# Optimization experiments

Measured on AMD Instinct MI355X. Metric: run time of the kernel, lower is better.

The kernel has to match this reference:

```python
import jax, jax.numpy as jnp
import numpy as np

N_SRC = 50000
N_DST = 50000
N_EDGES = 800000
D = 128
H = 128


def setup_inputs() -> dict:
    key = jax.random.key(0)
    ks = jax.random.split(key, 10)
    return {
        "feat_src": jax.random.normal(ks[0], (N_SRC, D), dtype=jnp.float32),
        "feat_dst": jax.random.normal(ks[1], (N_DST, D), dtype=jnp.float32),
        "W1": jax.random.normal(ks[2], (H, D), dtype=jnp.float32) * 0.05,
        "b1": jnp.zeros((H,), dtype=jnp.float32),
        "W2": jax.random.normal(ks[3], (H, 3 * D), dtype=jnp.float32) * 0.05,
        "b2": jnp.zeros((H,), dtype=jnp.float32),
        "W3": jax.random.normal(ks[4], (H, 2 * H), dtype=jnp.float32) * 0.05,
        "b3": jnp.zeros((H,), dtype=jnp.float32),
        "src_idx": jax.random.randint(ks[5], (N_EDGES,), 0, N_SRC, dtype=jnp.int32),
        "dst_idx": jax.random.randint(ks[6], (N_EDGES,), 0, N_DST, dtype=jnp.int32),
    }


def reference(feat_src, feat_dst, W1, b1, W2, b2, W3, b3, src_idx, dst_idx):
    n_dst = feat_dst.shape[0]
    # copy_u: gather source features along edges  [E, D]
    m = feat_src[src_idx]
    # fn.max -> 'max'; NOTE: source code's 'mean' is ALSO fn.max (faithful to bug)
    mx = jax.ops.segment_max(m, dst_idx, num_segments=n_dst)
    mx = jnp.where(jnp.isfinite(mx), mx, jnp.zeros_like(mx))  # zero-degree dst -> 0 (DGL convention)
    sm = jax.ops.segment_sum(m, dst_idx, num_segments=n_dst)
    agg = jnp.concatenate([mx, mx, sm], axis=1)  # [N_dst, 3D]
    z2 = agg @ W2.T + b2            # fc2
    z1 = feat_dst @ W1.T + b1       # fc1
    h = jax.nn.relu(jnp.concatenate([z2, z1], axis=1))  # [N_dst, 2H]
    out = jax.nn.relu(h @ W3.T + b3)  # fc3 = Linear + ReLU
    return out
```

## Files before the change

### kernel.cpp

```cpp
#include <hip/hip_runtime.h>
#include <math.h>

#define NDST 50000
#define NSRC 50000
#define NEDGE 800000
#define DF 128

#define NBUK 1563
#define NCH 128
#define EPC (NEDGE / NCH)
#define HN (NBUK * NCH)
#define CAP 1536

typedef __attribute__((ext_vector_type(4))) float f32x4;
typedef __attribute__((ext_vector_type(8))) short bf16x8;

__device__ __forceinline__ ushort f2bf(float f) {
    union { float f; unsigned int u; } c; c.f = f;
    unsigned int u = c.u;
    unsigned int r = (u + 0x7fffu + ((u >> 16) & 1u)) >> 16;
    return (ushort)r;
}
__device__ __forceinline__ float bflo(unsigned int u) {
    union { unsigned int u; float f; } c; c.u = u << 16; return c.f;
}
__device__ __forceinline__ float bfhi(unsigned int u) {
    union { unsigned int u; float f; } c; c.u = u & 0xffff0000u; return c.f;
}

#define NB_CONV 6250
#define NB_CONVD 6250
#define NB_ZERO 196
#define NB_PREP 320

__global__ void prep_all(const float* __restrict__ fs, unsigned int* __restrict__ fs_b,
                         const float* __restrict__ fd, unsigned int* __restrict__ fd_b,
                         uint4* __restrict__ hist4,
                         const float* __restrict__ W2, const float* __restrict__ W1,
                         const float* __restrict__ W3,
                         ushort* __restrict__ Wz_b, ushort* __restrict__ W1_b,
                         ushort* __restrict__ W3_b) {
    int b = blockIdx.x, tid = threadIdx.x;
    if (b < NB_CONV + NB_CONVD) {
        const float* src = (b < NB_CONV) ? fs : fd;
        unsigned int* dst = (b < NB_CONV) ? fs_b : fd_b;
        int i = ((b < NB_CONV) ? b : b - NB_CONV) * 256 + tid;
        float4 v = *(const float4*)(src + (size_t)i * 4);
        unsigned int lo = (unsigned int)f2bf(v.x) | ((unsigned int)f2bf(v.y) << 16);
        unsigned int hi = (unsigned int)f2bf(v.z) | ((unsigned int)f2bf(v.w) << 16);
        *(uint2*)(dst + (size_t)i * 2) = make_uint2(lo, hi);
    } else if (b < NB_CONV + NB_CONVD + NB_ZERO) {
        int i = (b - NB_CONV - NB_CONVD) * 256 + tid;
        if (i < HN / 4) hist4[i] = make_uint4(0, 0, 0, 0);
    } else {
        int i = (b - NB_CONV - NB_CONVD - NB_ZERO) * 256 + tid;
        if (i < 128 * 256) {
            int c = i >> 8, k = i & 255;
            float v = (k < 128) ? (W2[c * 384 + k] + W2[c * 384 + 128 + k])
                                : W2[c * 384 + 128 + k];
            Wz_b[i] = f2bf(v);
        } else if (i < 128 * 256 + 128 * 128) {
            int j = i - 128 * 256;
            W1_b[j] = f2bf(W1[j]);
        } else if (i < 128 * 256 + 128 * 128 + 128 * 256) {
            int j = i - 128 * 256 - 128 * 128;
            W3_b[j] = f2bf(W3[j]);
        }
    }
}

__global__ void hist_k(const int* __restrict__ dst_idx, int* __restrict__ hist) {
    int c = blockIdx.x, tid = threadIdx.x;
    int base = c * EPC;
    for (int e = base + tid; e < base + EPC; e += 256)
        atomicAdd(&hist[(dst_idx[e] >> 5) * NCH + c], 1);
}

__global__ void scan_bsums(const int* __restrict__ a, int* __restrict__ bsum, int n) {
    __shared__ int ws[4];
    int i = blockIdx.x * 256 + threadIdx.x;
    int v = (i < n) ? a[i] : 0;
    #pragma unroll
    for (int off = 32; off > 0; off >>= 1) v += __shfl_down(v, off, 64);
    if ((threadIdx.x & 63) == 0) ws[threadIdx.x >> 6] = v;
    __syncthreads();
    if (threadIdx.x == 0) bsum[blockIdx.x] = ws[0] + ws[1] + ws[2] + ws[3];
}

__global__ __launch_bounds__(256)
void scan_mid(const int* __restrict__ bsum, int* __restrict__ bpre, int nb) {
    __shared__ int part[256];
    int t = threadIdx.x;
    int ch = (nb + 255) / 256;
    int lo = t * ch, hi = min(nb, lo + ch);
    int s = 0;
    for (int i = lo; i < hi; ++i) s += bsum[i];
    part[t] = s;
    __syncthreads();
    for (int off = 1; off < 256; off <<= 1) {
        int v = (t >= off) ? part[t - off] : 0;
        __syncthreads();
        part[t] += v;
        __syncthreads();
    }
    int run = (t == 0) ? 0 : part[t - 1];
    for (int i = lo; i < hi; ++i) { bpre[i] = run; run += bsum[i]; }
}

__global__ __launch_bounds__(256)
void scan_final(const int* __restrict__ a, const int* __restrict__ bpre,
                int* __restrict__ out, int n) {
    __shared__ int s[256];
    int b = blockIdx.x, t = threadIdx.x;
    int i = b * 256 + t;
    int v = (i < n) ? a[i] : 0;
    s[t] = v;
    __syncthreads();
    for (int off = 1; off < 256; off <<= 1) {
        int u = (t >= off) ? s[t - off] : 0;
        __syncthreads();
        s[t] += u;
        __syncthreads();
    }
    if (i < n) out[i] = bpre[b] + s[t] - v;
}

__global__ __launch_bounds__(256)
void partition_k(const int* __restrict__ src_idx, const int* __restrict__ dst_idx,
                 const int* __restrict__ scanned, unsigned int* __restrict__ pairs) {
    __shared__ int offs_l[NBUK];
    int c = blockIdx.x, tid = threadIdx.x;
    for (int i = tid; i < NBUK; i += 256) offs_l[i] = scanned[i * NCH + c];
    __syncthreads();
    int base = c * EPC;
    for (int e = base + tid; e < base + EPC; e += 256) {
        int d = dst_idx[e];
        int pos = atomicAdd(&offs_l[d >> 5], 1);
        pairs[pos] = (unsigned int)src_idx[e] | ((unsigned int)(d & 31) << 16);
    }
}

__global__ __launch_bounds__(256)
void bucket_sort_agg(const unsigned int* __restrict__ fs_b,
                     const unsigned int* __restrict__ pairs,
                     const int* __restrict__ scanned,
                     unsigned int* __restrict__ mx_b, unsigned int* __restrict__ sm_b) {
    __shared__ int s_src[CAP];
    __shared__ int s_cnt[32], s_off[32], s_cur[32];
    int B = blockIdx.x, tid = threadIdx.x;
    int w = tid >> 6, lane = tid & 63;
    int s0 = scanned[B * NCH];
    int s1 = (B + 1 < NBUK) ? scanned[(B + 1) * NCH] : NEDGE;

    float mx0[8], mx1[8], sm0[8], sm1[8];
    #pragma unroll
    for (int j = 0; j < 8; ++j) {
        mx0[j] = -INFINITY; mx1[j] = -INFINITY; sm0[j] = 0.f; sm1[j] = 0.f;
    }

    for (int cs = s0; cs < s1; cs += CAP) {
        int n = min(CAP, s1 - cs);
        if (tid < 32) s_cnt[tid] = 0;
        __syncthreads();
        for (int i = tid; i < n; i += 256)
            atomicAdd(&s_cnt[(pairs[cs + i] >> 16) & 31u], 1);
        __syncthreads();
        if (tid < 32) {
            int v = s_cnt[tid];
            int incl = v;
            #pragma unroll
            for (int d = 1; d < 32; d <<= 1) {
                int o = __shfl_up(incl, d, 64);
                if (tid >= d) incl += o;
            }
            s_off[tid] = incl - v;
            s_cur[tid] = incl - v;
        }
        __syncthreads();
        for (int i = tid; i < n; i += 256) {
            unsigned int p = pairs[cs + i];
            int pos = atomicAdd(&s_cur[(p >> 16) & 31u], 1);
            s_src[pos] = (int)(p & 0xFFFFu);
        }
        __syncthreads();
        #pragma unroll
        for (int j = 0; j < 8; ++j) {
            int dl = w * 8 + j;
            int e = s_off[dl], eend = e + s_cnt[dl];
            for (; e + 3 < eend; e += 4) {
                int i0 = s_src[e], i1 = s_src[e + 1], i2 = s_src[e + 2], i3 = s_src[e + 3];
                unsigned int u0 = fs_b[(size_t)i0 * 64 + lane];
                unsigned int u1 = fs_b[(size_t)i1 * 64 + lane];
                unsigned int u2 = fs_b[(size_t)i2 * 64 + lane];
                unsigned int u3 = fs_b[(size_t)i3 * 64 + lane];
                float a0 = bflo(u0), c0 = bfhi(u0);
                float a1 = bflo(u1), c1 = bfhi(u1);
                float a2 = bflo(u2), c2 = bfhi(u2);
                float a3 = bflo(u3), c3 = bfhi(u3);
                mx0[j] = fmaxf(fmaxf(fmaxf(mx0[j], a0), a1), fmaxf(a2, a3));
                mx1[j] = fmaxf(fmaxf(fmaxf(mx1[j], c0), c1), fmaxf(c2, c3));
                sm0[j] += (a0 + a1) + (a2 + a3);
                sm1[j] += (c0 + c1) + (c2 + c3);
            }
            for (; e < eend; ++e) {
                unsigned int u = fs_b[(size_t)s_src[e] * 64 + lane];
                float a = bflo(u), c = bfhi(u);
                mx0[j] = fmaxf(mx0[j], a);
                mx1[j] = fmaxf(mx1[j], c);
                sm0[j] += a;
                sm1[j] += c;
            }
        }
        __syncthreads();
    }

    int base_d = B * 32;
    #pragma unroll
    for (int j = 0; j < 8; ++j) {
        int d = base_d + w * 8 + j;
        if (d >= NDST) continue;
        float m0 = mx0[j], m1 = mx1[j];
        if (m0 == -INFINITY) m0 = 0.f;
        if (m1 == -INFINITY) m1 = 0.f;
        union { float f; unsigned int u; } c0, c1;
        c0.f = m0; c1.f = m1;
        size_t o = (size_t)d * 64 + lane;
        mx_b[o] = (c0.u >> 16) | (c1.u & 0xFFFF0000u);
        sm_b[o] = (unsigned int)f2bf(sm0[j]) | ((unsigned int)f2bf(sm1[j]) << 16);
    }
}

#define BM2 64
#define LDH 260

__global__ __launch_bounds__(256)
void mlp_fused(const ushort* __restrict__ mxa, const ushort* __restrict__ sma,
               const ushort* __restrict__ fdb,
               const ushort* __restrict__ Wz_b, const ushort* __restrict__ W1_b,
               const ushort* __restrict__ W3_b,
               const float* __restrict__ b1, const float* __restrict__ b2,
               const float* __restrict__ b3,
               float* __restrict__ out) {
    __shared__ ushort Hs[BM2 * LDH];
    int tid = threadIdx.x;
    int bm = blockIdx.x * BM2;
    int wid = tid >> 6, lane = tid & 63;
    int wm = (wid & 1) * 32, wn = (wid >> 1) * 64;
    int lrow = lane & 15, lk8 = (lane >> 4) * 8;
    int rbase = (lane >> 4) * 4;

    int am0 = min(bm + wm + lrow, NDST - 1);
    int am1 = min(bm + wm + 16 + lrow, NDST - 1);
    int bn[4];
    #pragma unroll
    for (int ni = 0; ni < 4; ++ni) bn[ni] = wn + ni * 16 + lrow;

    f32x4 acc[2][4];

    #pragma unroll
    for (int i = 0; i < 2; ++i)
        #pragma unroll
        for (int j = 0; j < 4; ++j) acc[i][j] = (f32x4){0.f, 0.f, 0.f, 0.f};
    #pragma unroll 2
    for (int k0 = 0; k0 < 256; k0 += 32) {
        const ushort* ap = (k0 < 128) ? mxa : sma;
        int kl = (k0 & 127) + lk8;
        bf16x8 af0 = *(const bf16x8*)(ap + (size_t)am0 * 128 + kl);
        bf16x8 af1 = *(const bf16x8*)(ap + (size_t)am1 * 128 + kl);
        #pragma unroll
        for (int ni = 0; ni < 4; ++ni) {
            bf16x8 bf = *(const bf16x8*)(Wz_b + (size_t)bn[ni] * 256 + k0 + lk8);
            acc[0][ni] = __builtin_amdgcn_mfma_f32_16x16x32_bf16(af0, bf, acc[0][ni], 0, 0, 0);
            acc[1][ni] = __builtin_amdgcn_mfma_f32_16x16x32_bf16(af1, bf, acc[1][ni], 0, 0, 0);
        }
    }
    #pragma unroll
    for (int ni = 0; ni < 4; ++ni) {
        float bv = b2[bn[ni]];
        #pragma unroll
        for (int mi = 0; mi < 2; ++mi)
            #pragma unroll
            for (int r = 0; r < 4; ++r)
                Hs[(wm + mi * 16 + rbase + r) * LDH + bn[ni]] =
                    f2bf(fmaxf(acc[mi][ni][r] + bv, 0.f));
    }

    #pragma unroll
    for (int i = 0; i < 2; ++i)
        #pragma unroll
        for (int j = 0; j < 4; ++j) acc[i][j] = (f32x4){0.f, 0.f, 0.f, 0.f};
    #pragma unroll 2
    for (int k0 = 0; k0 < 128; k0 += 32) {
        bf16x8 af0 = *(const bf16x8*)(fdb + (size_t)am0 * 128 + k0 + lk8);
        bf16x8 af1 = *(const bf16x8*)(fdb + (size_t)am1 * 128 + k0 + lk8);
        #pragma unroll
        for (int ni = 0; ni < 4; ++ni) {
            bf16x8 bf = *(const bf16x8*)(W1_b + (size_t)bn[ni] * 128 + k0 + lk8);
            acc[0][ni] = __builtin_amdgcn_mfma_f32_16x16x32_bf16(af0, bf, acc[0][ni], 0, 0, 0);
            acc[1][ni] = __builtin_amdgcn_mfma_f32_16x16x32_bf16(af1, bf, acc[1][ni], 0, 0, 0);
        }
    }
    #pragma unroll
    for (int ni = 0; ni < 4; ++ni) {
        float bv = b1[bn[ni]];
        #pragma unroll
        for (int mi = 0; mi < 2; ++mi)
            #pragma unroll
            for (int r = 0; r < 4; ++r)
                Hs[(wm + mi * 16 + rbase + r) * LDH + 128 + bn[ni]] =
                    f2bf(fmaxf(acc[mi][ni][r] + bv, 0.f));
    }

    __syncthreads();

    #pragma unroll
    for (int i = 0; i < 2; ++i)
        #pragma unroll
        for (int j = 0; j < 4; ++j) acc[i][j] = (f32x4){0.f, 0.f, 0.f, 0.f};
    #pragma unroll 2
    for (int k0 = 0; k0 < 256; k0 += 32) {
        bf16x8 af0 = *(const bf16x8*)&Hs[(wm + lrow) * LDH + k0 + lk8];
        bf16x8 af1 = *(const bf16x8*)&Hs[(wm + 16 + lrow) * LDH + k0 + lk8];
        #pragma unroll
        for (int ni = 0; ni < 4; ++ni) {
            bf16x8 bf = *(const bf16x8*)(W3_b + (size_t)bn[ni] * 256 + k0 + lk8);
            acc[0][ni] = __builtin_amdgcn_mfma_f32_16x16x32_bf16(af0, bf, acc[0][ni], 0, 0, 0);
            acc[1][ni] = __builtin_amdgcn_mfma_f32_16x16x32_bf16(af1, bf, acc[1][ni], 0, 0, 0);
        }
    }
    #pragma unroll
    for (int ni = 0; ni < 4; ++ni) {
        float bv = b3[bn[ni]];
        #pragma unroll
        for (int mi = 0; mi < 2; ++mi)
            #pragma unroll
            for (int r = 0; r < 4; ++r) {
                int m = bm + wm + mi * 16 + rbase + r;
                if (m < NDST)
                    out[(size_t)m * 128 + bn[ni]] = fmaxf(acc[mi][ni][r] + bv, 0.f);
            }
    }
}

extern "C" void kernel_launch(void* const* d_in, const int* in_sizes, int n_in,
                              void* d_out, int out_size, void* d_ws, size_t ws_size,
                              hipStream_t stream) {
    const float* feat_src = (const float*)d_in[0];
    const float* feat_dst = (const float*)d_in[1];
    const float* W1 = (const float*)d_in[2];
    const float* b1 = (const float*)d_in[3];
    const float* W2 = (const float*)d_in[4];
    const float* b2 = (const float*)d_in[5];
    const float* W3 = (const float*)d_in[6];
    const float* b3 = (const float*)d_in[7];
    const int* src_idx = (const int*)d_in[8];
    const int* dst_idx = (const int*)d_in[9];

    float* out = (float*)d_out;

    unsigned int* fs_b = (unsigned int*)d_ws;
    unsigned int* mx_b = fs_b + (size_t)NSRC * 64;
    unsigned int* sm_b = mx_b + (size_t)NDST * 64;
    unsigned int* fd_b = sm_b + (size_t)NDST * 64;
    ushort* Wz_b = (ushort*)(fd_b + (size_t)NDST * 64);
    ushort* W1_b = Wz_b + 128 * 256;
    ushort* W3_b = W1_b + 128 * 128;
    int* hist    = (int*)(W3_b + 128 * 256);
    int* scanned = hist + HN;
    int* bsum    = scanned + HN;
    int* bpre    = bsum + 1024;
    unsigned int* pairs = (unsigned int*)(bpre + 1024);

    const int NBH = (HN + 255) / 256;

    prep_all<<<NB_CONV + NB_CONVD + NB_ZERO + NB_PREP, 256, 0, stream>>>(
        feat_src, fs_b, feat_dst, fd_b, (uint4*)hist, W2, W1, W3, Wz_b, W1_b, W3_b);

    hist_k<<<NCH, 256, 0, stream>>>(dst_idx, hist);
    scan_bsums<<<NBH, 256, 0, stream>>>(hist, bsum, HN);
    scan_mid<<<1, 256, 0, stream>>>(bsum, bpre, NBH);
    scan_final<<<NBH, 256, 0, stream>>>(hist, bpre, scanned, HN);
    partition_k<<<NCH, 256, 0, stream>>>(src_idx, dst_idx, scanned, pairs);

    bucket_sort_agg<<<NBUK, 256, 0, stream>>>(fs_b, pairs, scanned, mx_b, sm_b);

    mlp_fused<<<(NDST + BM2 - 1) / BM2, 256, 0, stream>>>(
        (const ushort*)mx_b, (const ushort*)sm_b, (const ushort*)fd_b,
        Wz_b, W1_b, W3_b, b1, b2, b3, out);
}
```

Before: 168.2 us.

## Stage MLP weight tiles through LDS with register double-buffered prefetch

Weight K-slices for the three GEMMs in the fused MLP kernel are now loaded cooperatively into a shared-memory tile, one 32-wide slice at a time. The next slice and the next A fragments are prefetched into registers while the current slice is used for MFMAs. This replaces per-wave redundant global loads of weights, which two waves each re-read, with one shared copy, and overlaps global latency with compute. In exchange it adds two block barriers per K step and extra LDS usage, which may lower occupancy.

```diff
diff --git a/kernel.cpp b/kernel.cpp
--- a/kernel.cpp
+++ b/kernel.cpp
@@ -232,6 +232,7 @@
 
 #define BM2 64
 #define LDH 260
+#define LDWS 40
 
 __global__ __launch_bounds__(256)
 void mlp_fused(const ushort* __restrict__ mxa, const ushort* __restrict__ sma,
@@ -242,6 +243,7 @@
                const float* __restrict__ b3,
                float* __restrict__ out) {
     __shared__ ushort Hs[BM2 * LDH];
+    __shared__ ushort Ws[128 * LDWS];
     int tid = threadIdx.x;
     int bm = blockIdx.x * BM2;
     int wid = tid >> 6, lane = tid & 63;
@@ -255,23 +257,45 @@
     #pragma unroll
     for (int ni = 0; ni < 4; ++ni) bn[ni] = wn + ni * 16 + lrow;
 
+    int srw = tid >> 1, skw = (tid & 1) * 16;
+    uint4 wr0, wr1;
+    bf16x8 a0[2], a1[2];
     f32x4 acc[2][4];
 
+#define STAGE_LOAD(Wb, K, k0) { const ushort* wp = (Wb) + (size_t)srw * (K) + (k0) + skw; \
+                                wr0 = *(const uint4*)wp; wr1 = *(const uint4*)(wp + 8); }
+#define STAGE_WRITE() { *(uint4*)&Ws[srw * LDWS + skw] = wr0; \
+                        *(uint4*)&Ws[srw * LDWS + skw + 8] = wr1; }
+
+    STAGE_LOAD(Wz_b, 256, 0);
+    a0[0] = *(const bf16x8*)(mxa + (size_t)am0 * 128 + lk8);
+    a1[0] = *(const bf16x8*)(mxa + (size_t)am1 * 128 + lk8);
+
     #pragma unroll
     for (int i = 0; i < 2; ++i)
         #pragma unroll
         for (int j = 0; j < 4; ++j) acc[i][j] = (f32x4){0.f, 0.f, 0.f, 0.f};
-    #pragma unroll 2
-    for (int k0 = 0; k0 < 256; k0 += 32) {
-        const ushort* ap = (k0 < 128) ? mxa : sma;
-        int kl = (k0 & 127) + lk8;
-        bf16x8 af0 = *(const bf16x8*)(ap + (size_t)am0 * 128 + kl);
-        bf16x8 af1 = *(const bf16x8*)(ap + (size_t)am1 * 128 + kl);
+    #pragma unroll
+    for (int k = 0; k < 8; ++k) {
+        if (k) __syncthreads();
+        STAGE_WRITE();
+        __syncthreads();
+        if (k < 7) { STAGE_LOAD(Wz_b, 256, (k + 1) * 32); }
+        else       { STAGE_LOAD(W1_b, 128, 0); }
+        if (k < 7) {
+            const ushort* ap = (k + 1 < 4) ? mxa : sma;
+            int kl = (((k + 1) * 32) & 127) + lk8;
+            a0[(k + 1) & 1] = *(const bf16x8*)(ap + (size_t)am0 * 128 + kl);
+            a1[(k + 1) & 1] = *(const bf16x8*)(ap + (size_t)am1 * 128 + kl);
+        } else {
+            a0[(k + 1) & 1] = *(const bf16x8*)(fdb + (size_t)am0 * 128 + lk8);
+            a1[(k + 1) & 1] = *(const bf16x8*)(fdb + (size_t)am1 * 128 + lk8);
+        }
         #pragma unroll
         for (int ni = 0; ni < 4; ++ni) {
-            bf16x8 bf = *(const bf16x8*)(Wz_b + (size_t)bn[ni] * 256 + k0 + lk8);
-            acc[0][ni] = __builtin_amdgcn_mfma_f32_16x16x32_bf16(af0, bf, acc[0][ni], 0, 0, 0);
-            acc[1][ni] = __builtin_amdgcn_mfma_f32_16x16x32_bf16(af1, bf, acc[1][ni], 0, 0, 0);
+            bf16x8 bf = *(const bf16x8*)&Ws[bn[ni] * LDWS + lk8];
+            acc[0][ni] = __builtin_amdgcn_mfma_f32_16x16x32_bf16(a0[k & 1], bf, acc[0][ni], 0, 0, 0);
+            acc[1][ni] = __builtin_amdgcn_mfma_f32_16x16x32_bf16(a1[k & 1], bf, acc[1][ni], 0, 0, 0);
         }
     }
     #pragma unroll
@@ -289,15 +313,23 @@
     for (int i = 0; i < 2; ++i)
         #pragma unroll
         for (int j = 0; j < 4; ++j) acc[i][j] = (f32x4){0.f, 0.f, 0.f, 0.f};
-    #pragma unroll 2
-    for (int k0 = 0; k0 < 128; k0 += 32) {
-        bf16x8 af0 = *(const bf16x8*)(fdb + (size_t)am0 * 128 + k0 + lk8);
-        bf16x8 af1 = *(const bf16x8*)(fdb + (size_t)am1 * 128 + k0 + lk8);
+    #pragma unroll
+    for (int k = 0; k < 4; ++k) {
+        __syncthreads();
+        STAGE_WRITE();
+        __syncthreads();
+        if (k < 3) { STAGE_LOAD(W1_b, 128, (k + 1) * 32); }
+        else       { STAGE_LOAD(W3_b, 256, 0); }
+        if (k < 3) {
+            int kl = (k + 1) * 32 + lk8;
+            a0[(k + 1) & 1] = *(const bf16x8*)(fdb + (size_t)am0 * 128 + kl);
+            a1[(k + 1) & 1] = *(const bf16x8*)(fdb + (size_t)am1 * 128 + kl);
+        }
         #pragma unroll
         for (int ni = 0; ni < 4; ++ni) {
-            bf16x8 bf = *(const bf16x8*)(W1_b + (size_t)bn[ni] * 128 + k0 + lk8);
-            acc[0][ni] = __builtin_amdgcn_mfma_f32_16x16x32_bf16(af0, bf, acc[0][ni], 0, 0, 0);
-            acc[1][ni] = __builtin_amdgcn_mfma_f32_16x16x32_bf16(af1, bf, acc[1][ni], 0, 0, 0);
+            bf16x8 bf = *(const bf16x8*)&Ws[bn[ni] * LDWS + lk8];
+            acc[0][ni] = __builtin_amdgcn_mfma_f32_16x16x32_bf16(a0[k & 1], bf, acc[0][ni], 0, 0, 0);
+            acc[1][ni] = __builtin_amdgcn_mfma_f32_16x16x32_bf16(a1[k & 1], bf, acc[1][ni], 0, 0, 0);
         }
     }
     #pragma unroll
@@ -311,19 +343,21 @@
                     f2bf(fmaxf(acc[mi][ni][r] + bv, 0.f));
     }
 
-    __syncthreads();
-
     #pragma unroll
     for (int i = 0; i < 2; ++i)
         #pragma unroll
         for (int j = 0; j < 4; ++j) acc[i][j] = (f32x4){0.f, 0.f, 0.f, 0.f};
-    #pragma unroll 2
-    for (int k0 = 0; k0 < 256; k0 += 32) {
-        bf16x8 af0 = *(const bf16x8*)&Hs[(wm + lrow) * LDH + k0 + lk8];
-        bf16x8 af1 = *(const bf16x8*)&Hs[(wm + 16 + lrow) * LDH + k0 + lk8];
+    #pragma unroll
+    for (int k = 0; k < 8; ++k) {
+        __syncthreads();
+        STAGE_WRITE();
+        __syncthreads();
+        if (k < 7) { STAGE_LOAD(W3_b, 256, (k + 1) * 32); }
+        bf16x8 af0 = *(const bf16x8*)&Hs[(wm + lrow) * LDH + k * 32 + lk8];
+        bf16x8 af1 = *(const bf16x8*)&Hs[(wm + 16 + lrow) * LDH + k * 32 + lk8];
         #pragma unroll
         for (int ni = 0; ni < 4; ++ni) {
-            bf16x8 bf = *(const bf16x8*)(W3_b + (size_t)bn[ni] * 256 + k0 + lk8);
+            bf16x8 bf = *(const bf16x8*)&Ws[bn[ni] * LDWS + lk8];
             acc[0][ni] = __builtin_amdgcn_mfma_f32_16x16x32_bf16(af0, bf, acc[0][ni], 0, 0, 0);
             acc[1][ni] = __builtin_amdgcn_mfma_f32_16x16x32_bf16(af1, bf, acc[1][ni], 0, 0, 0);
         }
@@ -340,6 +374,8 @@
                     out[(size_t)m * 128 + bn[ni]] = fmaxf(acc[mi][ni][r] + bv, 0.f);
             }
     }
+#undef STAGE_LOAD
+#undef STAGE_WRITE
 }
 
 extern "C" void kernel_launch(void* const* d_in, const int* in_sizes, int n_in,
```

Measured after the change: 150.4 us. -10.6%, faster.
